# Performance work log

Measured on AMD Instinct MI355X. Metric: run time of the kernel, lower is better.

The kernel has to match this reference:

```python
import jax, jax.numpy as jnp
import numpy as np

B, S, D, H, DH, L, FF = 1, 4096, 1536, 12, 128, 512, 8960
BLK = 64  # VSA cube size (4x4x4 tokens)
EPS = 1e-6


def _ln(x, eps=EPS):
    m = x.mean(-1, keepdims=True)
    v = ((x - m) ** 2).mean(-1, keepdims=True)
    return (x - m) * jax.lax.rsqrt(v + eps)


def _rms(x, w, eps=EPS):
    return x * jax.lax.rsqrt((x * x).mean(-1, keepdims=True) + eps) * w


def _rope(x, cos, sin):
    # x: [B,S,H,DH]; cos/sin: [S,DH//2]; non-neox (interleaved pairs)
    x1, x2 = x[..., ::2], x[..., 1::2]
    c, s = cos[None, :, None, :], sin[None, :, None, :]
    o1 = x1 * c - x2 * s
    o2 = x2 * c + x1 * s
    return jnp.stack([o1, o2], axis=-1).reshape(x.shape)


def _vsa(q, k, v, g, topk):
    # Video Sparse Attention: compressed (cube-mean) branch gated by g plus
    # block-sparse fine branch over top-k cubes selected from compressed probs.
    b, s, h, dh = q.shape
    nb = s // BLK
    scale = dh ** -0.5
    def blk(x):
        return x.reshape(b, nb, BLK, h, dh).transpose(0, 3, 1, 2, 4)  # [B,H,nb,BLK,DH]
    qb, kb, vb, gb = blk(q), blk(k), blk(v), blk(g)
    qc, kc, vc = qb.mean(3), kb.mean(3), vb.mean(3)  # [B,H,nb,DH]
    p = jax.nn.softmax(jnp.einsum('bhid,bhjd->bhij', qc, kc) * scale, axis=-1)
    oc = jnp.einsum('bhij,bhjd->bhid', p, vc)
    out_c = oc[:, :, :, None, :] * gb  # gate_compress applied per token
    _, idx = jax.lax.top_k(p, topk)  # [B,H,nb,topk]
    gather = jax.vmap(jax.vmap(lambda xb, ib: xb[ib]))  # over B,H
    k_sel = gather(kb, idx).reshape(b, h, nb, topk * BLK, dh)
    v_sel = gather(vb, idx).reshape(b, h, nb, topk * BLK, dh)
    pf = jax.nn.softmax(jnp.einsum('bhiqd,bhikd->bhiqk', qb, k_sel) * scale, axis=-1)
    of = jnp.einsum('bhiqk,bhikd->bhiqd', pf, v_sel)
    out = of + out_c  # [B,H,nb,BLK,DH]
    return out.transpose(0, 2, 3, 1, 4).reshape(b, s, h, dh)


def _forward(hidden_states, encoder_hidden_states, temb, cos, sin, sst,
             Wq, bq, Wk, bk, Wv, bv, Wg, bg, Wo, bo, nq_w, nk_w, ln1_w, ln1_b,
             cWq, cbq, cWk, cbk, cWv, cbv, cWo, cbo, cnq_w, cnk_w,
             W1, b1, W2, b2, topk):
    h_in = hidden_states
    e = sst + temb  # [1,6,D]
    shift, scale, gate, c_shift, c_scale, c_gate = [e[:, i:i + 1] for i in range(6)]
    norm1 = _ln(h_in) * (1.0 + scale) + shift
    q = _rms(norm1 @ Wq + bq, nq_w)
    k = _rms(norm1 @ Wk + bk, nk_w)
    v = norm1 @ Wv + bv
    g = norm1 @ Wg + bg
    q = q.reshape(B, S, H, DH); k = k.reshape(B, S, H, DH)
    v = v.reshape(B, S, H, DH); g = g.reshape(B, S, H, DH)
    q = _rope(q, cos, sin); k = _rope(k, cos, sin)
    attn = _vsa(q, k, v, g, topk).reshape(B, S, D)
    attn = attn @ Wo + bo
    resid1 = h_in + attn * gate
    norm2 = _ln(resid1) * ln1_w + ln1_b  # affine LN before cross-attn
    # T2V cross attention
    cq = _rms(norm2 @ cWq + cbq, cnq_w).reshape(B, S, H, DH)
    ck = _rms(encoder_hidden_states @ cWk + cbk, cnk_w).reshape(B, L, H, DH)
    cv = (encoder_hidden_states @ cWv + cbv).reshape(B, L, H, DH)
    sc = jnp.einsum('bqhd,bkhd->bhqk', cq, ck) * (DH ** -0.5)
    cout = jnp.einsum('bhqk,bkhd->bqhd', jax.nn.softmax(sc, axis=-1), cv)
    cout = cout.reshape(B, S, D) @ cWo + cbo
    resid2 = resid1 + cout
    norm3 = _ln(resid2) * (1.0 + c_scale) + c_shift
    ff = jax.nn.gelu(norm3 @ W1 + b1, approximate=True) @ W2 + b2
    return resid2 + ff * c_gate


def setup_inputs() -> dict:
    key = jax.random.key(0)
    ks = jax.random.split(key, 32)
    wi = 0.02
    def w(i, shp, s=wi):
        return jax.random.normal(ks[i], shp, dtype=jnp.float32) * s
    inp = {
        'hidden_states': jax.random.normal(ks[0], (B, S, D), dtype=jnp.float32),
        'encoder_hidden_states': jax.random.normal(ks[1], (B, L, D), dtype=jnp.float32),
        'temb': jax.random.normal(ks[2], (B, 6, D), dtype=jnp.float32),
        'cos': jax.random.uniform(ks[3], (S, DH // 2), dtype=jnp.float32),
        'sin': jax.random.uniform(ks[4], (S, DH // 2), dtype=jnp.float32),
        'sst': jax.random.normal(ks[5], (1, 6, D), dtype=jnp.float32) / (D ** 0.5),
        'Wq': w(6, (D, D)), 'bq': jnp.zeros((D,), jnp.float32),
        'Wk': w(7, (D, D)), 'bk': jnp.zeros((D,), jnp.float32),
        'Wv': w(8, (D, D)), 'bv': jnp.zeros((D,), jnp.float32),
        'Wg': w(9, (D, D)), 'bg': jnp.zeros((D,), jnp.float32),
        'Wo': w(10, (D, D)), 'bo': jnp.zeros((D,), jnp.float32),
        'nq_w': jnp.ones((D,), jnp.float32), 'nk_w': jnp.ones((D,), jnp.float32),
        'ln1_w': jnp.ones((D,), jnp.float32), 'ln1_b': jnp.zeros((D,), jnp.float32),
        'cWq': w(11, (D, D)), 'cbq': jnp.zeros((D,), jnp.float32),
        'cWk': w(12, (D, D)), 'cbk': jnp.zeros((D,), jnp.float32),
        'cWv': w(13, (D, D)), 'cbv': jnp.zeros((D,), jnp.float32),
        'cWo': w(14, (D, D)), 'cbo': jnp.zeros((D,), jnp.float32),
        'cnq_w': jnp.ones((D,), jnp.float32), 'cnk_w': jnp.ones((D,), jnp.float32),
        'W1': w(15, (D, FF)), 'b1': jnp.zeros((FF,), jnp.float32),
        'W2': w(16, (FF, D)), 'b2': jnp.zeros((D,), jnp.float32),
        'topk': 8,
    }
    return inp


def reference(hidden_states, encoder_hidden_states, temb, cos, sin, sst,
              Wq, bq, Wk, bk, Wv, bv, Wg, bg, Wo, bo, nq_w, nk_w, ln1_w, ln1_b,
              cWq, cbq, cWk, cbk, cWv, cbv, cWo, cbo, cnq_w, cnk_w,
              W1, b1, W2, b2, topk):
    return _forward(hidden_states, encoder_hidden_states, temb, cos, sin, sst,
                    Wq, bq, Wk, bk, Wv, bv, Wg, bg, Wo, bo, nq_w, nk_w, ln1_w, ln1_b,
                    cWq, cbq, cWk, cbk, cWv, cbv, cWo, cbo, cnq_w, cnk_w,
                    W1, b1, W2, b2, topk)
```

## Files before the change

kernel.cpp:

```cpp
#include <hip/hip_runtime.h>
#include <math.h>


namespace {
constexpr int S_   = 4096;
constexpr int D_   = 1536;
constexpr int H_   = 12;
constexpr int L_   = 512;
constexpr int TOPK = 8;
constexpr int FF_  = 8960;
constexpr float EPS_   = 1e-6f;
constexpr float SCALE_ = 0.08838834764831845f;
}

typedef __attribute__((ext_vector_type(8))) short short8;
typedef __attribute__((ext_vector_type(4))) float f32x4;

#define AS_GLOBAL __attribute__((address_space(1)))
#define AS_LDS    __attribute__((address_space(3)))

__device__ __forceinline__ short f2bf(float x) {
    uint32_t u = __float_as_uint(x);
    uint32_t r = (u + 0x7FFFu + ((u >> 16) & 1u)) >> 16;
    return (short)r;
}
__device__ __forceinline__ float bf2f(short s) {
    return __uint_as_float(((uint32_t)(uint16_t)s) << 16);
}
__device__ __forceinline__ float gelu_tanh(float x) {
    const float t = tanhf(0.7978845608028654f * (x + 0.044715f * x * x * x));
    return 0.5f * x * (1.f + t);
}

__device__ __forceinline__ float block_sum_256(float v, float* red) {
#pragma unroll
    for (int off = 32; off > 0; off >>= 1) v += __shfl_down(v, off, 64);
    const int lane = threadIdx.x & 63, w = threadIdx.x >> 6;
    if (lane == 0) red[w] = v;
    __syncthreads();
    v = red[0] + red[1] + red[2] + red[3];
    __syncthreads();
    return v;
}

template <int EPI>
__global__ __launch_bounds__(256, 2) void gemm12(
    const short* __restrict__ A, const short* __restrict__ Bt,
    const float* __restrict__ bias, float* __restrict__ C,
    short* __restrict__ Cb, int M, int N, int K,
    const float* __restrict__ Rres, const float* __restrict__ gate)
{
    __shared__ __align__(16) short As[2][128 * 64];
    __shared__ __align__(16) short Bs[2][128 * 64];
    const int tid = threadIdx.x;
    const int wid = tid >> 6, lane = tid & 63;
    const int wm = wid >> 1, wn = wid & 1;
    const int g16 = lane >> 4, l15 = lane & 15;

    const int gx = gridDim.x;
    const int nwg = gx * gridDim.y;
    const int bid = blockIdx.y * gx + blockIdx.x;
    const int qq = nwg >> 3, r8 = nwg & 7;
    const int xcd = bid & 7, lid = bid >> 3;
    const int swz = ((xcd < r8) ? xcd * (qq + 1) : r8 * (qq + 1) + (xcd - r8) * qq) + lid;
    const int stripe = swz / (4 * gx);
    const int within = swz - stripe * (4 * gx);
    const int m0 = (stripe * 4 + (within & 3)) * 128;
    const int n0 = (within >> 2) * 128;

    f32x4 acc[4][4];
#pragma unroll
    for (int i = 0; i < 4; i++)
#pragma unroll
        for (int j = 0; j < 4; j++) acc[i][j] = (f32x4){0.f, 0.f, 0.f, 0.f};

    int sr[4], su[4];
#pragma unroll
    for (int i = 0; i < 4; i++) {
        const int c = tid + 256 * i;
        sr[i] = c >> 3;
        su[i] = (c & 7) ^ (sr[i] & 7);
    }

    auto STAGE = [&](int buf, int kt) {
#pragma unroll
        for (int i = 0; i < 4; i++)
            __builtin_amdgcn_global_load_lds(
                (const AS_GLOBAL short*)(A + (size_t)(m0 + sr[i]) * K + kt + su[i] * 8),
                (AS_LDS short*)(&As[buf][(tid + 256 * i) * 8]), 16, 0, 0);
#pragma unroll
        for (int i = 0; i < 4; i++)
            __builtin_amdgcn_global_load_lds(
                (const AS_GLOBAL short*)(Bt + (size_t)(n0 + sr[i]) * K + kt + su[i] * 8),
                (AS_LDS short*)(&Bs[buf][(tid + 256 * i) * 8]), 16, 0, 0);
    };

    const int nk = K >> 6;
    STAGE(0, 0);

    int cur = 0;
    for (int t = 0; t < nk; ++t) {
        if (t + 1 < nk) {
            STAGE(cur ^ 1, (t + 1) << 6);
            asm volatile("s_waitcnt vmcnt(8)" ::: "memory");
        } else {
            asm volatile("s_waitcnt vmcnt(0)" ::: "memory");
        }
        __builtin_amdgcn_s_barrier();
        __builtin_amdgcn_sched_barrier(0);

        short8 a[4][2], b[4][2];
#pragma unroll
        for (int mi = 0; mi < 4; mi++) {
            const int row = wm * 64 + mi * 16 + l15;
#pragma unroll
            for (int kk = 0; kk < 2; kk++) {
                const int u = (kk * 4 + g16) ^ (row & 7);
                a[mi][kk] = *(const short8*)(As[cur] + row * 64 + u * 8);
            }
        }
#pragma unroll
        for (int ni = 0; ni < 4; ni++) {
            const int row = wn * 64 + ni * 16 + l15;
#pragma unroll
            for (int kk = 0; kk < 2; kk++) {
                const int u = (kk * 4 + g16) ^ (row & 7);
                b[ni][kk] = *(const short8*)(Bs[cur] + row * 64 + u * 8);
            }
        }
        asm volatile("s_waitcnt lgkmcnt(0)" ::: "memory");
        __builtin_amdgcn_sched_barrier(0);
        __builtin_amdgcn_s_barrier();
        __builtin_amdgcn_sched_barrier(0);

        __builtin_amdgcn_s_setprio(1);
#pragma unroll
        for (int mi = 0; mi < 4; mi++)
#pragma unroll
            for (int ni = 0; ni < 4; ni++)
#pragma unroll
                for (int kk = 0; kk < 2; kk++)
                    acc[mi][ni] = __builtin_amdgcn_mfma_f32_16x16x32_bf16(
                        a[mi][kk], b[ni][kk], acc[mi][ni], 0, 0, 0);
        __builtin_amdgcn_s_setprio(0);

        cur ^= 1;
    }

    const size_t SD = (size_t)S_ * D_;
#pragma unroll
    for (int mi = 0; mi < 4; mi++) {
#pragma unroll
        for (int ni = 0; ni < 4; ni++) {
            const int col = n0 + wn * 64 + ni * 16 + l15;
            const float bv = bias[col];
#pragma unroll
            for (int rr = 0; rr < 4; rr++) {
                const int row = m0 + wm * 64 + mi * 16 + g16 * 4 + rr;
                const float v = acc[mi][ni][rr];
                if (EPI == 4) {
                    const int seg = col / 1536, cl = col - seg * 1536;
                    const float y = v + bv;
                    if (seg < 2) C[(size_t)seg * SD + (size_t)row * 1536 + cl] = y;
                    else Cb[(size_t)(seg - 2) * SD + (size_t)row * 1536 + cl] = f2bf(y);
                } else {
                    const size_t o = (size_t)row * N + col;
                    if (EPI == 0) C[o] = v + bv;
                    else if (EPI == 2) Cb[o] = f2bf(gelu_tanh(v + bv));
                    else if (EPI == 3) Cb[o] = f2bf(v + bv);
                    else if (EPI == 6) C[o] = Rres[o] + (v + bv) * gate[col];
                    else if (EPI == 7) C[o] += v + bv;
                }
            }
        }
    }
}

__global__ __launch_bounds__(256) void transpose_w(
    const float* __restrict__ W, short* __restrict__ Th, int Kd, int Nd)
{
    __shared__ float tile[64][65];
    const int k0 = blockIdx.y * 64, n0 = blockIdx.x * 64;
    for (int f = threadIdx.x; f < 1024; f += 256) {
        const int rr = f >> 4, c4 = (f & 15) * 4;
        const float4 v = *(const float4*)(W + (size_t)(k0 + rr) * Nd + n0 + c4);
        tile[rr][c4 + 0] = v.x; tile[rr][c4 + 1] = v.y;
        tile[rr][c4 + 2] = v.z; tile[rr][c4 + 3] = v.w;
    }
    __syncthreads();
    for (int f = threadIdx.x; f < 1024; f += 256) {
        const int nn = f >> 4, k4 = (f & 15) * 4;
        short4 hv;
        hv.x = f2bf(tile[k4 + 0][nn]); hv.y = f2bf(tile[k4 + 1][nn]);
        hv.z = f2bf(tile[k4 + 2][nn]); hv.w = f2bf(tile[k4 + 3][nn]);
        *(short4*)(Th + (size_t)(n0 + nn) * Kd + k0 + k4) = hv;
    }
}

__global__ void cvt_bf16_kernel(const float* __restrict__ x, short* __restrict__ y, int n4)
{
    const int i = blockIdx.x * 256 + threadIdx.x;
    if (i >= n4) return;
    const float4 v = *(const float4*)(x + (size_t)i * 4);
    short4 o; o.x = f2bf(v.x); o.y = f2bf(v.y); o.z = f2bf(v.z); o.w = f2bf(v.w);
    *(short4*)(y + (size_t)i * 4) = o;
}

__global__ void fill_bcat(const float* __restrict__ bq, const float* __restrict__ bk,
                          const float* __restrict__ bv, const float* __restrict__ bg,
                          float* __restrict__ bcat)
{
    const int i = blockIdx.x * 256 + threadIdx.x;
    if (i >= 6144) return;
    const int seg = i / 1536, c = i - seg * 1536;
    const float* src = (seg == 0) ? bq : (seg == 1) ? bk : (seg == 2) ? bv : bg;
    bcat[i] = src[c];
}

template <int ADD1>
__global__ __launch_bounds__(256) void ln_bf16(
    const float* __restrict__ x, short* __restrict__ hi,
    const float* __restrict__ g, const float* __restrict__ b)
{
    __shared__ float red[4];
    const size_t s = blockIdx.x;
    const float* xr = x + s * D_;
    float v[6];
    float sm = 0.f;
#pragma unroll
    for (int i = 0; i < 6; i++) { v[i] = xr[threadIdx.x + 256 * i]; sm += v[i]; }
    sm = block_sum_256(sm, red);
    const float mean = sm * (1.f / D_);
    float vs = 0.f;
#pragma unroll
    for (int i = 0; i < 6; i++) { const float d = v[i] - mean; vs += d * d; }
    vs = block_sum_256(vs, red);
    const float rs = rsqrtf(vs * (1.f / D_) + EPS_);
#pragma unroll
    for (int i = 0; i < 6; i++) {
        const int d = threadIdx.x + 256 * i;
        hi[s * D_ + d] = f2bf((v[i] - mean) * rs * (g[d] + (float)ADD1) + b[d]);
    }
}

__global__ __launch_bounds__(256) void rms_kernel(float* __restrict__ x,
                                                  const float* __restrict__ w)
{
    __shared__ float red[4];
    const size_t s = blockIdx.x;
    float* xr = x + s * D_;
    float v[6];
    float ss = 0.f;
#pragma unroll
    for (int i = 0; i < 6; i++) { v[i] = xr[threadIdx.x + 256 * i]; ss += v[i] * v[i]; }
    ss = block_sum_256(ss, red);
    const float rs = rsqrtf(ss * (1.f / D_) + EPS_);
#pragma unroll
    for (int i = 0; i < 6; i++) {
        const int d = threadIdx.x + 256 * i;
        xr[d] = v[i] * rs * w[d];
    }
}

__global__ __launch_bounds__(256) void rmsrope_qk(
    float* __restrict__ Q, float* __restrict__ K,
    const float* __restrict__ nqw, const float* __restrict__ nkw,
    const float* __restrict__ cosT, const float* __restrict__ sinT)
{
    __shared__ float red[4];
    const size_t s = blockIdx.x;
    const int tid = threadIdx.x;

#pragma unroll
    for (int m = 0; m < 2; m++) {
        float* X = m ? K : Q;
        const float* w = m ? nkw : nqw;
        float2 v[3];
        float ss = 0.f;
#pragma unroll
        for (int j = 0; j < 3; j++) {
            v[j] = *(const float2*)(X + s * D_ + 2 * (tid + 256 * j));
            ss += v[j].x * v[j].x + v[j].y * v[j].y;
        }
        ss = block_sum_256(ss, red);
        const float rs = rsqrtf(ss * (1.f / D_) + EPS_);
#pragma unroll
        for (int j = 0; j < 3; j++) {
            const int p = tid + 256 * j;
            const int i = p & 63;
            const float c = cosT[s * 64 + i], sn = sinT[s * 64 + i];
            const float x1 = v[j].x * rs * w[2 * p];
            const float x2 = v[j].y * rs * w[2 * p + 1];
            float2 o;
            o.x = x1 * c - x2 * sn;
            o.y = x2 * c + x1 * sn;
            *(float2*)(X + s * D_ + 2 * p) = o;
        }
    }
}

__global__ void add_kernel(const float* __restrict__ a, const float* __restrict__ b,
                           float* __restrict__ o, int n)
{
    const int i = blockIdx.x * 256 + threadIdx.x;
    if (i < n) o[i] = a[i] + b[i];
}

__global__ __launch_bounds__(128) void blockmean_f32(const float* __restrict__ q,
                                                     float* __restrict__ qc)
{
    const int hb = blockIdx.x;
    const int h = hb >> 6, j = hb & 63;
    const int d = threadIdx.x;
    float sum = 0.f;
    for (int t = 0; t < 64; t++)
        sum += q[(size_t)(j * 64 + t) * D_ + h * 128 + d];
    qc[(size_t)hb * 128 + d] = sum * (1.f / 64.f);
}

__global__ __launch_bounds__(128) void blockmean_bf16(const short* __restrict__ q,
                                                      float* __restrict__ qc)
{
    const int hb = blockIdx.x;
    const int h = hb >> 6, j = hb & 63;
    const int d = threadIdx.x;
    float sum = 0.f;
    for (int t = 0; t < 64; t++)
        sum += bf2f(q[(size_t)(j * 64 + t) * D_ + h * 128 + d]);
    qc[(size_t)hb * 128 + d] = sum * (1.f / 64.f);
}

__global__ __launch_bounds__(64) void coarse_kernel(
    const float* __restrict__ qc, const float* __restrict__ kc,
    const float* __restrict__ vc, float* __restrict__ oc, int* __restrict__ idxout)
{
    const int hb = blockIdx.x;
    const int h = hb >> 6, i = hb & 63;
    const int lane = threadIdx.x;
    __shared__ float p[64];

    const float* qv = qc + (size_t)hb * 128;
    const float* kv = kc + (size_t)((h << 6) + lane) * 128;
    float sc = 0.f;
    for (int d = 0; d < 128; d++) sc = fmaf(qv[d], kv[d], sc);
    sc *= SCALE_;

    float mx = sc;
#pragma unroll
    for (int off = 32; off > 0; off >>= 1) mx = fmaxf(mx, __shfl_xor(mx, off, 64));
    const float e = expf(sc - mx);
    float sumv = e;
#pragma unroll
    for (int off = 32; off > 0; off >>= 1) sumv += __shfl_xor(sumv, off, 64);
    const float pv = e / sumv;
    p[lane] = pv;
    __syncthreads();

    float o0 = 0.f, o1 = 0.f;
    for (int j = 0; j < 64; j++) {
        const float pj = p[j];
        const float* vr = vc + (size_t)((h << 6) + j) * 128;
        o0 = fmaf(pj, vr[lane], o0);
        o1 = fmaf(pj, vr[lane + 64], o1);
    }
    oc[(size_t)hb * 128 + lane]      = o0;
    oc[(size_t)hb * 128 + lane + 64] = o1;

    float v = pv;
    for (int t = 0; t < TOPK; t++) {
        float bv = v; int bi = lane;
#pragma unroll
        for (int off = 32; off > 0; off >>= 1) {
            const float ov = __shfl_xor(bv, off, 64);
            const int   oi = __shfl_xor(bi, off, 64);
            if (ov > bv || (ov == bv && oi < bi)) { bv = ov; bi = oi; }
        }
        if (lane == 0) idxout[hb * TOPK + t] = bi;
        if (lane == bi) v = -1.f;
    }
}

template <int MODE>
__global__ __launch_bounds__(256) void attn_mfma(
    const float* __restrict__ Qf, const float* __restrict__ Kf,
    const short* __restrict__ Vbb, const float* __restrict__ Vff,
    const short* __restrict__ Gb, const float* __restrict__ ocp,
    const int* __restrict__ idxp, short* __restrict__ Ob)
{
    const int hb = blockIdx.x, h = hb >> 6, ib = hb & 63;
    const int tid = threadIdx.x, wid = tid >> 6, lane = tid & 63;
    const int g16 = lane >> 4, l15 = lane & 15;

    __shared__ __align__(16) short Ks[64 * 128];
    __shared__ __align__(16) short Vst[128 * 64];
    __shared__ __align__(16) short Ps[64 * 80];
    __shared__ int sel[8];
    if (tid < 8) sel[tid] = (MODE == 0) ? idxp[hb * 8 + tid] : tid;

    short8 qa[4];
    {
        const float* qrow = Qf + (size_t)(ib * 64 + wid * 16 + l15) * D_ + h * 128;
#pragma unroll
        for (int kk = 0; kk < 4; kk++) {
            const float4 f0 = *(const float4*)(qrow + kk * 32 + g16 * 8);
            const float4 f1 = *(const float4*)(qrow + kk * 32 + g16 * 8 + 4);
            short8 v;
            v[0] = f2bf(f0.x); v[1] = f2bf(f0.y); v[2] = f2bf(f0.z); v[3] = f2bf(f0.w);
            v[4] = f2bf(f1.x); v[5] = f2bf(f1.y); v[6] = f2bf(f1.z); v[7] = f2bf(f1.w);
            qa[kk] = v;
        }
    }

    f32x4 o[8];
#pragma unroll
    for (int n2 = 0; n2 < 8; n2++) o[n2] = (f32x4){0.f, 0.f, 0.f, 0.f};
    float mrow[4] = {-3e38f, -3e38f, -3e38f, -3e38f};
    float lrow[4] = {0.f, 0.f, 0.f, 0.f};
    __syncthreads();

    for (int t = 0; t < 8; t++) {
        const int jb = sel[t];
#pragma unroll
        for (int it = 0; it < 4; it++) {
            const int c = tid + 256 * it;
            const int key = c >> 4, d8 = (c & 15) * 8;
            const float* src = Kf + (size_t)(jb * 64 + key) * D_ + h * 128 + d8;
            const float4 f0 = *(const float4*)src;
            const float4 f1 = *(const float4*)(src + 4);
            short8 v;
            v[0] = f2bf(f0.x); v[1] = f2bf(f0.y); v[2] = f2bf(f0.z); v[3] = f2bf(f0.w);
            v[4] = f2bf(f1.x); v[5] = f2bf(f1.y); v[6] = f2bf(f1.z); v[7] = f2bf(f1.w);
            const int byte = (key * 256 + d8 * 2) ^ ((key & 7) << 4);
            *(short8*)((char*)Ks + byte) = v;
        }
#pragma unroll
        for (int it = 0; it < 4; it++) {
            const int c = tid + 256 * it;
            const int key = c & 63, d8 = (c >> 6) * 8;
            float vv[8];
            if (MODE == 0) {
                const short8 v = *(const short8*)(Vbb + (size_t)(jb * 64 + key) * D_ + h * 128 + d8);
#pragma unroll
                for (int j = 0; j < 8; j++) vv[j] = bf2f(v[j]);
            } else {
                const float* src = Vff + (size_t)(jb * 64 + key) * D_ + h * 128 + d8;
                const float4 f0 = *(const float4*)src;
                const float4 f1 = *(const float4*)(src + 4);
                vv[0] = f0.x; vv[1] = f0.y; vv[2] = f0.z; vv[3] = f0.w;
                vv[4] = f1.x; vv[5] = f1.y; vv[6] = f1.z; vv[7] = f1.w;
            }
#pragma unroll
            for (int j = 0; j < 8; j++) {
                const int dim = d8 + j;
                const int byte = (dim * 128 + key * 2) ^ ((dim & 7) << 4);
                *(short*)((char*)Vst + byte) = f2bf(vv[j]);
            }
        }
        __syncthreads();

        f32x4 s[4];
#pragma unroll
        for (int nt = 0; nt < 4; nt++) {
            f32x4 acc = (f32x4){0.f, 0.f, 0.f, 0.f};
            const int key = nt * 16 + l15;
#pragma unroll
            for (int kk = 0; kk < 4; kk++) {
                const int byte = (key * 256 + (kk * 32 + g16 * 8) * 2) ^ ((key & 7) << 4);
                const short8 b = *(const short8*)((char*)Ks + byte);
                acc = __builtin_amdgcn_mfma_f32_16x16x32_bf16(qa[kk], b, acc, 0, 0, 0);
            }
            s[nt] = acc;
        }
#pragma unroll
        for (int nt = 0; nt < 4; nt++)
#pragma unroll
            for (int rr = 0; rr < 4; rr++) s[nt][rr] *= SCALE_;

        float alpha[4];
#pragma unroll
        for (int rr = 0; rr < 4; rr++) {
            float v = fmaxf(fmaxf(s[0][rr], s[1][rr]), fmaxf(s[2][rr], s[3][rr]));
            v = fmaxf(v, __shfl_xor(v, 1, 64));
            v = fmaxf(v, __shfl_xor(v, 2, 64));
            v = fmaxf(v, __shfl_xor(v, 4, 64));
            v = fmaxf(v, __shfl_xor(v, 8, 64));
            const float mn = fmaxf(mrow[rr], v);
            alpha[rr] = expf(mrow[rr] - mn);
            mrow[rr] = mn;
        }
        float rs[4] = {0.f, 0.f, 0.f, 0.f};
#pragma unroll
        for (int nt = 0; nt < 4; nt++)
#pragma unroll
            for (int rr = 0; rr < 4; rr++) {
                const float p = expf(s[nt][rr] - mrow[rr]);
                s[nt][rr] = p;
                rs[rr] += p;
            }
#pragma unroll
        for (int rr = 0; rr < 4; rr++) {
            float v = rs[rr];
            v += __shfl_xor(v, 1, 64);
            v += __shfl_xor(v, 2, 64);
            v += __shfl_xor(v, 4, 64);
            v += __shfl_xor(v, 8, 64);
            lrow[rr] = lrow[rr] * alpha[rr] + v;
        }
#pragma unroll
        for (int n2 = 0; n2 < 8; n2++)
#pragma unroll
            for (int rr = 0; rr < 4; rr++) o[n2][rr] *= alpha[rr];

#pragma unroll
        for (int nt = 0; nt < 4; nt++)
#pragma unroll
            for (int rr = 0; rr < 4; rr++)
                Ps[(wid * 16 + g16 * 4 + rr) * 80 + nt * 16 + l15] = f2bf(s[nt][rr]);

#pragma unroll
        for (int kk2 = 0; kk2 < 2; kk2++) {
            const short8 pa = *(const short8*)(Ps + (wid * 16 + l15) * 80 + kk2 * 32 + g16 * 8);
#pragma unroll
            for (int n2 = 0; n2 < 8; n2++) {
                const int dim = n2 * 16 + l15;
                const int byte = (dim * 128 + (kk2 * 32 + g16 * 8) * 2) ^ ((dim & 7) << 4);
                const short8 vb = *(const short8*)((char*)Vst + byte);
                o[n2] = __builtin_amdgcn_mfma_f32_16x16x32_bf16(pa, vb, o[n2], 0, 0, 0);
            }
        }
        __syncthreads();
    }

#pragma unroll
    for (int n2 = 0; n2 < 8; n2++) {
        const int col = n2 * 16 + l15;
        const float ocv = (MODE == 0) ? ocp[(size_t)hb * 128 + col] : 0.f;
#pragma unroll
        for (int rr = 0; rr < 4; rr++) {
            const int row = ib * 64 + wid * 16 + g16 * 4 + rr;
            float val = o[n2][rr] / lrow[rr];
            if (MODE == 0)
                val += ocv * bf2f(Gb[(size_t)row * D_ + h * 128 + col]);
            Ob[(size_t)row * D_ + h * 128 + col] = f2bf(val);
        }
    }
}

extern "C" void kernel_launch(void* const* d_in, const int* in_sizes, int n_in,
                              void* d_out, int out_size, void* d_ws, size_t ws_size,
                              hipStream_t stream)
{
    const float* h_in = (const float*)d_in[0];
    const float* enc  = (const float*)d_in[1];
    const float* temb = (const float*)d_in[2];
    const float* cosT = (const float*)d_in[3];
    const float* sinT = (const float*)d_in[4];
    const float* sst  = (const float*)d_in[5];
    const float* Wq = (const float*)d_in[6];   const float* bq = (const float*)d_in[7];
    const float* Wk = (const float*)d_in[8];   const float* bk = (const float*)d_in[9];
    const float* Wv = (const float*)d_in[10];  const float* bv = (const float*)d_in[11];
    const float* Wg = (const float*)d_in[12];  const float* bg = (const float*)d_in[13];
    const float* Wo = (const float*)d_in[14];  const float* bo = (const float*)d_in[15];
    const float* nq_w  = (const float*)d_in[16];
    const float* nk_w  = (const float*)d_in[17];
    const float* ln1_w = (const float*)d_in[18];
    const float* ln1_b = (const float*)d_in[19];
    const float* cWq = (const float*)d_in[20]; const float* cbq = (const float*)d_in[21];
    const float* cWk = (const float*)d_in[22]; const float* cbk = (const float*)d_in[23];
    const float* cWv = (const float*)d_in[24]; const float* cbv = (const float*)d_in[25];
    const float* cWo = (const float*)d_in[26]; const float* cbo = (const float*)d_in[27];
    const float* cnq_w = (const float*)d_in[28];
    const float* cnk_w = (const float*)d_in[29];
    const float* W1 = (const float*)d_in[30];  const float* b1 = (const float*)d_in[31];
    const float* W2 = (const float*)d_in[32];  const float* b2 = (const float*)d_in[33];
    float* out = (float*)d_out;

    char* base = (char*)d_ws;
    size_t off = 0;
    auto alloc = [&](size_t bytes) {
        char* p = base + off;
        off += (bytes + 255) & ~(size_t)255;
        return p;
    };
    const size_t SD = (size_t)S_ * D_;
    float* e_   = (float*)alloc(6 * D_ * 4);
    float* Q_   = (float*)alloc(SD * 4);
    float* K_   = (float*)alloc(SD * 4);
    float* CK_  = (float*)alloc((size_t)L_ * D_ * 4);
    float* CV_  = (float*)alloc((size_t)L_ * D_ * 4);
    float* qc_  = (float*)alloc((size_t)H_ * 64 * 128 * 4);
    float* kc_  = (float*)alloc((size_t)H_ * 64 * 128 * 4);
    float* vc_  = (float*)alloc((size_t)H_ * 64 * 128 * 4);
    float* oc_  = (float*)alloc((size_t)H_ * 64 * 128 * 4);
    int*   idx_ = (int*)alloc((size_t)H_ * 64 * TOPK * 4);
    short* Nb   = (short*)alloc(SD * 2);
    short* Vb   = (short*)alloc(SD * 2);
    short* Gb   = (short*)alloc(SD * 2);
    short* attn_b = (short*)alloc(SD * 2);
    short* enc_b  = (short*)alloc((size_t)L_ * D_ * 2);
    const size_t WDD = (size_t)D_ * D_;
    short* Wqt = (short*)alloc(WDD * 2);
    short* Wkt = (short*)alloc(WDD * 2);
    short* Wvt = (short*)alloc(WDD * 2);
    short* Wgt = (short*)alloc(WDD * 2);
    short* Wot = (short*)alloc(WDD * 2);
    short* cWqt = (short*)alloc(WDD * 2); short* cWkt = (short*)alloc(WDD * 2);
    short* cWvt = (short*)alloc(WDD * 2); short* cWot = (short*)alloc(WDD * 2);
    short* W1t = (short*)alloc((size_t)D_ * FF_ * 2);
    short* W2t = (short*)alloc((size_t)D_ * FF_ * 2);
    float* bcat = (float*)alloc(6144 * 4);
    short* FFC = Vb;

    const dim3 b256(256);
    const int nSD = S_ * D_;
    const dim3 gDD(D_ / 64, D_ / 64);
    const dim3 gN1536(D_ / 128, S_ / 128);

    add_kernel<<<dim3((6 * D_ + 255) / 256), b256, 0, stream>>>(sst, temb, e_, 6 * D_);
    ln_bf16<1><<<dim3(S_), b256, 0, stream>>>(h_in, Nb, e_ + D_, e_);
    fill_bcat<<<dim3(24), b256, 0, stream>>>(bq, bk, bv, bg, bcat);

    transpose_w<<<gDD, b256, 0, stream>>>(Wq, Wqt, D_, D_);
    transpose_w<<<gDD, b256, 0, stream>>>(Wk, Wkt, D_, D_);
    transpose_w<<<gDD, b256, 0, stream>>>(Wv, Wvt, D_, D_);
    transpose_w<<<gDD, b256, 0, stream>>>(Wg, Wgt, D_, D_);
    transpose_w<<<gDD, b256, 0, stream>>>(Wo, Wot, D_, D_);
    transpose_w<<<gDD, b256, 0, stream>>>(cWq, cWqt, D_, D_);
    transpose_w<<<gDD, b256, 0, stream>>>(cWk, cWkt, D_, D_);
    transpose_w<<<gDD, b256, 0, stream>>>(cWv, cWvt, D_, D_);
    transpose_w<<<gDD, b256, 0, stream>>>(cWo, cWot, D_, D_);
    transpose_w<<<dim3(FF_ / 64, D_ / 64), b256, 0, stream>>>(W1, W1t, D_, FF_);
    transpose_w<<<dim3(D_ / 64, FF_ / 64), b256, 0, stream>>>(W2, W2t, FF_, D_);
    cvt_bf16_kernel<<<dim3((L_ * D_ / 4 + 255) / 256), b256, 0, stream>>>(enc, enc_b, L_ * D_ / 4);

    gemm12<4><<<dim3(6144 / 128, S_ / 128), b256, 0, stream>>>(
        Nb, Wqt, bcat, Q_, Vb, S_, 6144, D_, nullptr, nullptr);

    rmsrope_qk<<<dim3(S_), b256, 0, stream>>>(Q_, K_, nq_w, nk_w, cosT, sinT);

    blockmean_f32<<<dim3(H_ * 64), dim3(128), 0, stream>>>(Q_, qc_);
    blockmean_f32<<<dim3(H_ * 64), dim3(128), 0, stream>>>(K_, kc_);
    blockmean_bf16<<<dim3(H_ * 64), dim3(128), 0, stream>>>(Vb, vc_);
    coarse_kernel<<<dim3(H_ * 64), dim3(64), 0, stream>>>(qc_, kc_, vc_, oc_, idx_);

    attn_mfma<0><<<dim3(H_ * 64), b256, 0, stream>>>(
        Q_, K_, Vb, nullptr, Gb, oc_, idx_, attn_b);

    gemm12<6><<<gN1536, b256, 0, stream>>>(attn_b, Wot, bo, K_, nullptr, S_, D_, D_,
                                           h_in, e_ + 2 * D_);

    ln_bf16<0><<<dim3(S_), b256, 0, stream>>>(K_, Nb, ln1_w, ln1_b);
    gemm12<0><<<gN1536, b256, 0, stream>>>(Nb, cWqt, cbq, Q_, nullptr, S_, D_, D_,
                                           nullptr, nullptr);
    rms_kernel<<<dim3(S_), b256, 0, stream>>>(Q_, cnq_w);

    const dim3 gLenc(D_ / 128, L_ / 128);
    gemm12<0><<<gLenc, b256, 0, stream>>>(enc_b, cWkt, cbk, CK_, nullptr, L_, D_, D_,
                                          nullptr, nullptr);
    rms_kernel<<<dim3(L_), b256, 0, stream>>>(CK_, cnk_w);
    gemm12<0><<<gLenc, b256, 0, stream>>>(enc_b, cWvt, cbv, CV_, nullptr, L_, D_, D_,
                                          nullptr, nullptr);

    attn_mfma<1><<<dim3(H_ * 64), b256, 0, stream>>>(
        Q_, CK_, nullptr, CV_, nullptr, nullptr, nullptr, attn_b);

    gemm12<7><<<gN1536, b256, 0, stream>>>(attn_b, cWot, cbo, K_, nullptr, S_, D_, D_,
                                           nullptr, nullptr);

    ln_bf16<1><<<dim3(S_), b256, 0, stream>>>(K_, Nb, e_ + 4 * D_, e_ + 3 * D_);
    gemm12<2><<<dim3(FF_ / 128, S_ / 128), b256, 0, stream>>>(
        Nb, W1t, b1, nullptr, FFC, S_, FF_, D_, nullptr, nullptr);
    gemm12<6><<<gN1536, b256, 0, stream>>>(FFC, W2t, b2, out, nullptr, S_, D_, FF_,
                                           K_, e_ + 5 * D_);
}
```

Before: 1.072 ms.

## Shrink GEMM N-tile to 64 and keep fused QKVG outputs in bf16

The GEMM tile changes from 128x128 to 128x64 with a smaller B LDS buffer and launch bounds raised to 3 blocks per CU. The aim is more workgroups on narrow-N GEMMs and better occupancy. Separately, the fused QKVG projection now writes Q and K as bf16 instead of fp32. RMS+RoPE, block-mean and sparse attention then read bf16 directly, which removes fp32 traffic and in-kernel conversions. The costs are lower per-tile reuse (more A reloads) and an extra bf16 rounding of Q/K before RMS norm, which may slightly affect accuracy.

```diff
diff --git a/kernel.cpp b/kernel.cpp
--- a/kernel.cpp
+++ b/kernel.cpp
@@ -44,14 +44,14 @@
 }
 
 template <int EPI>
-__global__ __launch_bounds__(256, 2) void gemm12(
+__global__ __launch_bounds__(256, 3) void gemm14(
     const short* __restrict__ A, const short* __restrict__ Bt,
     const float* __restrict__ bias, float* __restrict__ C,
     short* __restrict__ Cb, int M, int N, int K,
     const float* __restrict__ Rres, const float* __restrict__ gate)
 {
     __shared__ __align__(16) short As[2][128 * 64];
-    __shared__ __align__(16) short Bs[2][128 * 64];
+    __shared__ __align__(16) short Bs[2][64 * 64];
     const int tid = threadIdx.x;
     const int wid = tid >> 6, lane = tid & 63;
     const int wm = wid >> 1, wn = wid & 1;
@@ -66,32 +66,38 @@
     const int stripe = swz / (4 * gx);
     const int within = swz - stripe * (4 * gx);
     const int m0 = (stripe * 4 + (within & 3)) * 128;
-    const int n0 = (within >> 2) * 128;
-
-    f32x4 acc[4][4];
+    const int n0 = (within >> 2) * 64;
+
+    f32x4 acc[4][2];
 #pragma unroll
     for (int i = 0; i < 4; i++)
 #pragma unroll
-        for (int j = 0; j < 4; j++) acc[i][j] = (f32x4){0.f, 0.f, 0.f, 0.f};
-
-    int sr[4], su[4];
+        for (int j = 0; j < 2; j++) acc[i][j] = (f32x4){0.f, 0.f, 0.f, 0.f};
+
+    int ar[4], au[4], br[2], bu[2];
 #pragma unroll
     for (int i = 0; i < 4; i++) {
         const int c = tid + 256 * i;
-        sr[i] = c >> 3;
-        su[i] = (c & 7) ^ (sr[i] & 7);
+        ar[i] = c >> 3;
+        au[i] = (c & 7) ^ (ar[i] & 7);
+    }
+#pragma unroll
+    for (int i = 0; i < 2; i++) {
+        const int c = tid + 256 * i;
+        br[i] = c >> 3;
+        bu[i] = (c & 7) ^ (br[i] & 7);
     }
 
     auto STAGE = [&](int buf, int kt) {
 #pragma unroll
         for (int i = 0; i < 4; i++)
             __builtin_amdgcn_global_load_lds(
-                (const AS_GLOBAL short*)(A + (size_t)(m0 + sr[i]) * K + kt + su[i] * 8),
+                (const AS_GLOBAL short*)(A + (size_t)(m0 + ar[i]) * K + kt + au[i] * 8),
                 (AS_LDS short*)(&As[buf][(tid + 256 * i) * 8]), 16, 0, 0);
 #pragma unroll
-        for (int i = 0; i < 4; i++)
+        for (int i = 0; i < 2; i++)
             __builtin_amdgcn_global_load_lds(
-                (const AS_GLOBAL short*)(Bt + (size_t)(n0 + sr[i]) * K + kt + su[i] * 8),
+                (const AS_GLOBAL short*)(Bt + (size_t)(n0 + br[i]) * K + kt + bu[i] * 8),
                 (AS_LDS short*)(&Bs[buf][(tid + 256 * i) * 8]), 16, 0, 0);
     };
 
@@ -102,14 +108,14 @@
     for (int t = 0; t < nk; ++t) {
         if (t + 1 < nk) {
             STAGE(cur ^ 1, (t + 1) << 6);
-            asm volatile("s_waitcnt vmcnt(8)" ::: "memory");
+            asm volatile("s_waitcnt vmcnt(6)" ::: "memory");
         } else {
             asm volatile("s_waitcnt vmcnt(0)" ::: "memory");
         }
         __builtin_amdgcn_s_barrier();
         __builtin_amdgcn_sched_barrier(0);
 
-        short8 a[4][2], b[4][2];
+        short8 a[4][2], b[2][2];
 #pragma unroll
         for (int mi = 0; mi < 4; mi++) {
             const int row = wm * 64 + mi * 16 + l15;
@@ -120,8 +126,8 @@
             }
         }
 #pragma unroll
-        for (int ni = 0; ni < 4; ni++) {
-            const int row = wn * 64 + ni * 16 + l15;
+        for (int ni = 0; ni < 2; ni++) {
+            const int row = wn * 32 + ni * 16 + l15;
 #pragma unroll
             for (int kk = 0; kk < 2; kk++) {
                 const int u = (kk * 4 + g16) ^ (row & 7);
@@ -137,7 +143,7 @@
 #pragma unroll
         for (int mi = 0; mi < 4; mi++)
 #pragma unroll
-            for (int ni = 0; ni < 4; ni++)
+            for (int ni = 0; ni < 2; ni++)
 #pragma unroll
                 for (int kk = 0; kk < 2; kk++)
                     acc[mi][ni] = __builtin_amdgcn_mfma_f32_16x16x32_bf16(
@@ -151,8 +157,8 @@
 #pragma unroll
     for (int mi = 0; mi < 4; mi++) {
 #pragma unroll
-        for (int ni = 0; ni < 4; ni++) {
-            const int col = n0 + wn * 64 + ni * 16 + l15;
+        for (int ni = 0; ni < 2; ni++) {
+            const int col = n0 + wn * 32 + ni * 16 + l15;
             const float bv = bias[col];
 #pragma unroll
             for (int rr = 0; rr < 4; rr++) {
@@ -160,14 +166,11 @@
                 const float v = acc[mi][ni][rr];
                 if (EPI == 4) {
                     const int seg = col / 1536, cl = col - seg * 1536;
-                    const float y = v + bv;
-                    if (seg < 2) C[(size_t)seg * SD + (size_t)row * 1536 + cl] = y;
-                    else Cb[(size_t)(seg - 2) * SD + (size_t)row * 1536 + cl] = f2bf(y);
+                    Cb[(size_t)seg * SD + (size_t)row * 1536 + cl] = f2bf(v + bv);
                 } else {
                     const size_t o = (size_t)row * N + col;
                     if (EPI == 0) C[o] = v + bv;
                     else if (EPI == 2) Cb[o] = f2bf(gelu_tanh(v + bv));
-                    else if (EPI == 3) Cb[o] = f2bf(v + bv);
                     else if (EPI == 6) C[o] = Rres[o] + (v + bv) * gate[col];
                     else if (EPI == 7) C[o] += v + bv;
                 }
@@ -262,8 +265,8 @@
     }
 }
 
-__global__ __launch_bounds__(256) void rmsrope_qk(
-    float* __restrict__ Q, float* __restrict__ K,
+__global__ __launch_bounds__(256) void rmsrope_qk_bf16(
+    short* __restrict__ Q, short* __restrict__ K,
     const float* __restrict__ nqw, const float* __restrict__ nkw,
     const float* __restrict__ cosT, const float* __restrict__ sinT)
 {
@@ -273,14 +276,15 @@
 
 #pragma unroll
     for (int m = 0; m < 2; m++) {
-        float* X = m ? K : Q;
+        short* X = m ? K : Q;
         const float* w = m ? nkw : nqw;
-        float2 v[3];
+        float v1[3], v2[3];
         float ss = 0.f;
 #pragma unroll
         for (int j = 0; j < 3; j++) {
-            v[j] = *(const float2*)(X + s * D_ + 2 * (tid + 256 * j));
-            ss += v[j].x * v[j].x + v[j].y * v[j].y;
+            const short2 p2 = *(const short2*)(X + s * D_ + 2 * (tid + 256 * j));
+            v1[j] = bf2f(p2.x); v2[j] = bf2f(p2.y);
+            ss += v1[j] * v1[j] + v2[j] * v2[j];
         }
         ss = block_sum_256(ss, red);
         const float rs = rsqrtf(ss * (1.f / D_) + EPS_);
@@ -289,12 +293,12 @@
             const int p = tid + 256 * j;
             const int i = p & 63;
             const float c = cosT[s * 64 + i], sn = sinT[s * 64 + i];
-            const float x1 = v[j].x * rs * w[2 * p];
-            const float x2 = v[j].y * rs * w[2 * p + 1];
-            float2 o;
-            o.x = x1 * c - x2 * sn;
-            o.y = x2 * c + x1 * sn;
-            *(float2*)(X + s * D_ + 2 * p) = o;
+            const float x1 = v1[j] * rs * w[2 * p];
+            const float x2 = v2[j] * rs * w[2 * p + 1];
+            short2 o;
+            o.x = f2bf(x1 * c - x2 * sn);
+            o.y = f2bf(x2 * c + x1 * sn);
+            *(short2*)(X + s * D_ + 2 * p) = o;
         }
     }
 }
@@ -304,18 +308,6 @@
 {
     const int i = blockIdx.x * 256 + threadIdx.x;
     if (i < n) o[i] = a[i] + b[i];
-}
-
-__global__ __launch_bounds__(128) void blockmean_f32(const float* __restrict__ q,
-                                                     float* __restrict__ qc)
-{
-    const int hb = blockIdx.x;
-    const int h = hb >> 6, j = hb & 63;
-    const int d = threadIdx.x;
-    float sum = 0.f;
-    for (int t = 0; t < 64; t++)
-        sum += q[(size_t)(j * 64 + t) * D_ + h * 128 + d];
-    qc[(size_t)hb * 128 + d] = sum * (1.f / 64.f);
 }
 
 __global__ __launch_bounds__(128) void blockmean_bf16(const short* __restrict__ q,
@@ -382,8 +374,10 @@
 
 template <int MODE>
 __global__ __launch_bounds__(256) void attn_mfma(
+    const short* __restrict__ Qb, const short* __restrict__ Kb,
+    const short* __restrict__ Vbb,
     const float* __restrict__ Qf, const float* __restrict__ Kf,
-    const short* __restrict__ Vbb, const float* __restrict__ Vff,
+    const float* __restrict__ Vff,
     const short* __restrict__ Gb, const float* __restrict__ ocp,
     const int* __restrict__ idxp, short* __restrict__ Ob)
 {
@@ -398,7 +392,12 @@
     if (tid < 8) sel[tid] = (MODE == 0) ? idxp[hb * 8 + tid] : tid;
 
     short8 qa[4];
-    {
+    if (MODE == 0) {
+        const short* qrow = Qb + (size_t)(ib * 64 + wid * 16 + l15) * D_ + h * 128;
+#pragma unroll
+        for (int kk = 0; kk < 4; kk++)
+            qa[kk] = *(const short8*)(qrow + kk * 32 + g16 * 8);
+    } else {
         const float* qrow = Qf + (size_t)(ib * 64 + wid * 16 + l15) * D_ + h * 128;
 #pragma unroll
         for (int kk = 0; kk < 4; kk++) {
@@ -423,15 +422,20 @@
 #pragma unroll
         for (int it = 0; it < 4; it++) {
             const int c = tid + 256 * it;
-            const int key = c >> 4, d8 = (c & 15) * 8;
-            const float* src = Kf + (size_t)(jb * 64 + key) * D_ + h * 128 + d8;
-            const float4 f0 = *(const float4*)src;
-            const float4 f1 = *(const float4*)(src + 4);
-            short8 v;
-            v[0] = f2bf(f0.x); v[1] = f2bf(f0.y); v[2] = f2bf(f0.z); v[3] = f2bf(f0.w);
-            v[4] = f2bf(f1.x); v[5] = f2bf(f1.y); v[6] = f2bf(f1.z); v[7] = f2bf(f1.w);
-            const int byte = (key * 256 + d8 * 2) ^ ((key & 7) << 4);
-            *(short8*)((char*)Ks + byte) = v;
+            const int key = c >> 4, u16 = c & 15;
+            const int byte = (key * 256 + u16 * 16) ^ ((key & 7) << 4);
+            if (MODE == 0) {
+                *(short8*)((char*)Ks + byte) =
+                    *(const short8*)(Kb + (size_t)(jb * 64 + key) * D_ + h * 128 + u16 * 8);
+            } else {
+                const float* src = Kf + (size_t)(jb * 64 + key) * D_ + h * 128 + u16 * 8;
+                const float4 f0 = *(const float4*)src;
+                const float4 f1 = *(const float4*)(src + 4);
+                short8 v;
+                v[0] = f2bf(f0.x); v[1] = f2bf(f0.y); v[2] = f2bf(f0.z); v[3] = f2bf(f0.w);
+                v[4] = f2bf(f1.x); v[5] = f2bf(f1.y); v[6] = f2bf(f1.z); v[7] = f2bf(f1.w);
+                *(short8*)((char*)Ks + byte) = v;
+            }
         }
 #pragma unroll
         for (int it = 0; it < 4; it++) {
@@ -594,8 +598,7 @@
     float* oc_  = (float*)alloc((size_t)H_ * 64 * 128 * 4);
     int*   idx_ = (int*)alloc((size_t)H_ * 64 * TOPK * 4);
     short* Nb   = (short*)alloc(SD * 2);
-    short* Vb   = (short*)alloc(SD * 2);
-    short* Gb   = (short*)alloc(SD * 2);
+    short* QKVGb = (short*)alloc(4 * SD * 2);
     short* attn_b = (short*)alloc(SD * 2);
     short* enc_b  = (short*)alloc((size_t)L_ * D_ * 2);
     const size_t WDD = (size_t)D_ * D_;
@@ -609,12 +612,15 @@
     short* W1t = (short*)alloc((size_t)D_ * FF_ * 2);
     short* W2t = (short*)alloc((size_t)D_ * FF_ * 2);
     float* bcat = (float*)alloc(6144 * 4);
-    short* FFC = Vb;
+    short* FFC = QKVGb;
+    short* Qb = QKVGb;
+    short* Kb = QKVGb + SD;
+    short* Vb = QKVGb + 2 * SD;
+    short* Gb = QKVGb + 3 * SD;
 
     const dim3 b256(256);
-    const int nSD = S_ * D_;
     const dim3 gDD(D_ / 64, D_ / 64);
-    const dim3 gN1536(D_ / 128, S_ / 128);
+    const dim3 gN1536(D_ / 64, S_ / 128);
 
     add_kernel<<<dim3((6 * D_ + 255) / 256), b256, 0, stream>>>(sst, temb, e_, 6 * D_);
     ln_bf16<1><<<dim3(S_), b256, 0, stream>>>(h_in, Nb, e_ + D_, e_);
@@ -633,43 +639,43 @@
     transpose_w<<<dim3(D_ / 64, FF_ / 64), b256, 0, stream>>>(W2, W2t, FF_, D_);
     cvt_bf16_kernel<<<dim3((L_ * D_ / 4 + 255) / 256), b256, 0, stream>>>(enc, enc_b, L_ * D_ / 4);
 
-    gemm12<4><<<dim3(6144 / 128, S_ / 128), b256, 0, stream>>>(
-        Nb, Wqt, bcat, Q_, Vb, S_, 6144, D_, nullptr, nullptr);
-
-    rmsrope_qk<<<dim3(S_), b256, 0, stream>>>(Q_, K_, nq_w, nk_w, cosT, sinT);
-
-    blockmean_f32<<<dim3(H_ * 64), dim3(128), 0, stream>>>(Q_, qc_);
-    blockmean_f32<<<dim3(H_ * 64), dim3(128), 0, stream>>>(K_, kc_);
+    gemm14<4><<<dim3(6144 / 64, S_ / 128), b256, 0, stream>>>(
+        Nb, Wqt, bcat, nullptr, QKVGb, S_, 6144, D_, nullptr, nullptr);
+
+    rmsrope_qk_bf16<<<dim3(S_), b256, 0, stream>>>(Qb, Kb, nq_w, nk_w, cosT, sinT);
+
+    blockmean_bf16<<<dim3(H_ * 64), dim3(128), 0, stream>>>(Qb, qc_);
+    blockmean_bf16<<<dim3(H_ * 64), dim3(128), 0, stream>>>(Kb, kc_);
     blockmean_bf16<<<dim3(H_ * 64), dim3(128), 0, stream>>>(Vb, vc_);
     coarse_kernel<<<dim3(H_ * 64), dim3(64), 0, stream>>>(qc_, kc_, vc_, oc_, idx_);
 
     attn_mfma<0><<<dim3(H_ * 64), b256, 0, stream>>>(
-        Q_, K_, Vb, nullptr, Gb, oc_, idx_, attn_b);
-
-    gemm12<6><<<gN1536, b256, 0, stream>>>(attn_b, Wot, bo, K_, nullptr, S_, D_, D_,
+        Qb, Kb, Vb, nullptr, nullptr, nullptr, Gb, oc_, idx_, attn_b);
+
+    gemm14<6><<<gN1536, b256, 0, stream>>>(attn_b, Wot, bo, K_, nullptr, S_, D_, D_,
                                            h_in, e_ + 2 * D_);
 
     ln_bf16<0><<<dim3(S_), b256, 0, stream>>>(K_, Nb, ln1_w, ln1_b);
-    gemm12<0><<<gN1536, b256, 0, stream>>>(Nb, cWqt, cbq, Q_, nullptr, S_, D_, D_,
+    gemm14<0><<<gN1536, b256, 0, stream>>>(Nb, cWqt, cbq, Q_, nullptr, S_, D_, D_,
                                            nullptr, nullptr);
     rms_kernel<<<dim3(S_), b256, 0, stream>>>(Q_, cnq_w);
 
-    const dim3 gLenc(D_ / 128, L_ / 128);
-    gemm12<0><<<gLenc, b256, 0, stream>>>(enc_b, cWkt, cbk, CK_, nullptr, L_, D_, D_,
+    const dim3 gLenc(D_ / 64, L_ / 128);
+    gemm14<0><<<gLenc, b256, 0, stream>>>(enc_b, cWkt, cbk, CK_, nullptr, L_, D_, D_,
                                           nullptr, nullptr);
     rms_kernel<<<dim3(L_), b256, 0, stream>>>(CK_, cnk_w);
-    gemm12<0><<<gLenc, b256, 0, stream>>>(enc_b, cWvt, cbv, CV_, nullptr, L_, D_, D_,
+    gemm14<0><<<gLenc, b256, 0, stream>>>(enc_b, cWvt, cbv, CV_, nullptr, L_, D_, D_,
                                           nullptr, nullptr);
 
     attn_mfma<1><<<dim3(H_ * 64), b256, 0, stream>>>(
-        Q_, CK_, nullptr, CV_, nullptr, nullptr, nullptr, attn_b);
-
-    gemm12<7><<<gN1536, b256, 0, stream>>>(attn_b, cWot, cbo, K_, nullptr, S_, D_, D_,
+        nullptr, nullptr, nullptr, Q_, CK_, CV_, nullptr, nullptr, nullptr, attn_b);
+
+    gemm14<7><<<gN1536, b256, 0, stream>>>(attn_b, cWot, cbo, K_, nullptr, S_, D_, D_,
                                            nullptr, nullptr);
 
     ln_bf16<1><<<dim3(S_), b256, 0, stream>>>(K_, Nb, e_ + 4 * D_, e_ + 3 * D_);
-    gemm12<2><<<dim3(FF_ / 128, S_ / 128), b256, 0, stream>>>(
+    gemm14<2><<<dim3(FF_ / 64, S_ / 128), b256, 0, stream>>>(
         Nb, W1t, b1, nullptr, FFC, S_, FF_, D_, nullptr, nullptr);
-    gemm12<6><<<gN1536, b256, 0, stream>>>(FFC, W2t, b2, out, nullptr, S_, D_, FF_,
+    gemm14<6><<<gN1536, b256, 0, stream>>>(FFC, W2t, b2, out, nullptr, S_, D_, FF_,
                                            K_, e_ + 5 * D_);
 }
```

Result: faster. 930.2 us (-13.2%).
